# Kernel tuning notes

Hardware: AMD Instinct MI355X
Metric: run time of the kernel (lower is better)

The kernel has to match this reference:

```python
import jax, jax.numpy as jnp
import numpy as np

B, S, DIM, H, DH = 2, 2048, 1024, 16, 64
EPS = 1e-6


def rms_norm(x, w):
    # x: (..., DH); computed in fp32 like the torch module
    norm = jax.lax.rsqrt(jnp.mean(jnp.square(x), axis=-1, keepdims=True) + EPS)
    return (x * norm) * w


def apply_rope(x, freqs):
    # x: (B, H, S, D), freqs: (S, D); torch code slices cos/sin to first half
    d = x.shape[-1] // 2
    cos = jnp.cos(freqs)[None, None, :, :d]
    sin = jnp.sin(freqs)[None, None, :, :d]
    x1, x2 = x[..., :d], x[..., d:]
    return jnp.concatenate([x1 * cos - x2 * sin, x2 * cos + x1 * sin], axis=-1)


def setup_inputs() -> dict:
    key = jax.random.key(0)
    ks = jax.random.split(key, 4)
    x = jax.random.normal(ks[0], (B, S, DIM), dtype=jnp.float32)
    # causal additive mask
    causal = jnp.tril(jnp.ones((S, S), dtype=bool))
    mask = jnp.where(causal, 0.0, -1e9).astype(jnp.float32)[None, None]
    # standard rope frequencies: pos * inv_freq over head_dim
    inv_freq = 1.0 / (10000.0 ** (jnp.arange(0, DH, dtype=jnp.float32) / DH))
    rope_freqs = jnp.arange(S, dtype=jnp.float32)[:, None] * inv_freq[None, :]
    total = H * DH
    w_qkv = jax.random.normal(ks[1], (3 * total, DIM), dtype=jnp.float32) * (DIM ** -0.5)
    w_out = jax.random.normal(ks[2], (DIM, total), dtype=jnp.float32) * (total ** -0.5)
    q_norm_w = jnp.ones((DH,), dtype=jnp.float32)
    k_norm_w = jnp.ones((DH,), dtype=jnp.float32)
    return {"x": x, "mask": mask, "rope_freqs": rope_freqs, "w_qkv": w_qkv,
            "w_out": w_out, "q_norm_w": q_norm_w, "k_norm_w": k_norm_w}


def reference(x, mask, rope_freqs, w_qkv, w_out, q_norm_w, k_norm_w):
    b, s, _ = x.shape
    qkv = (x @ w_qkv.T).reshape(b, s, 3, H, DH)
    q, k, v = qkv[:, :, 0], qkv[:, :, 1], qkv[:, :, 2]
    q = jnp.transpose(rms_norm(q, q_norm_w), (0, 2, 1, 3))  # (B,H,S,DH)
    k = jnp.transpose(rms_norm(k, k_norm_w), (0, 2, 1, 3))
    v = jnp.transpose(v, (0, 2, 1, 3))
    q = apply_rope(q, rope_freqs)
    k = apply_rope(k, rope_freqs)
    scale = DH ** -0.5
    attn = jnp.einsum('bhsd,bhtd->bhst', q, k) * scale + mask
    attn = jax.nn.softmax(attn, axis=-1)
    out = jnp.einsum('bhst,bhtd->bhsd', attn, v)
    out = jnp.transpose(out, (0, 2, 1, 3)).reshape(b, s, H * DH)
    return out @ w_out.T
```

## Files before the change

### kernel.cpp

```cpp
#include <hip/hip_runtime.h>
#include <hip/hip_bf16.h>
#include <stdint.h>

typedef short bf16x8 __attribute__((ext_vector_type(8)));
typedef float f32x4  __attribute__((ext_vector_type(4)));

#define MFMA_BF16(a,b,c) __builtin_amdgcn_mfma_f32_16x16x32_bf16((a),(b),(c),0,0,0)

__device__ __forceinline__ void async_ld16(const void* g, void* l) {
  __builtin_amdgcn_global_load_lds(
      (const __attribute__((address_space(1))) void*)g,
      (__attribute__((address_space(3))) void*)l, 16, 0, 0);
}

__device__ __forceinline__ unsigned short bf16_bits(float x) {
  __hip_bfloat16 h = __float2bfloat16(x);
  return *(unsigned short*)&h;
}

#define NX_C    (2 * 2048 * 1024)
#define NWQKV_C (3072 * 1024)
#define NWOUT_C (1024 * 1024)

__global__ void __launch_bounds__(256)
cvt_all(const float* __restrict__ x, const float* __restrict__ wqkv,
        const float* __restrict__ wout, __hip_bfloat16* __restrict__ dst)
{
  const int i = (blockIdx.x * 256 + threadIdx.x) * 4;
  const float* src;
  int off;
  if (i < NX_C)                { src = x;    off = i; }
  else if (i < NX_C + NWQKV_C) { src = wqkv; off = i - NX_C; }
  else                         { src = wout; off = i - NX_C - NWQKV_C; }
  const float4 v = *(const float4*)(src + off);
  ushort4 u;
  u.x = bf16_bits(v.x); u.y = bf16_bits(v.y);
  u.z = bf16_bits(v.z); u.w = bf16_bits(v.w);
  *(ushort4*)((unsigned short*)dst + i) = u;
}

template<int EPI>
__global__ void __launch_bounds__(256)
gemm_bt(const __hip_bfloat16* __restrict__ A,
        const __hip_bfloat16* __restrict__ B,
        int K,
        __hip_bfloat16* __restrict__ o0,
        __hip_bfloat16* __restrict__ o1,
        __hip_bfloat16* __restrict__ o2,
        float* __restrict__ of)
{
  __shared__ __align__(16) __hip_bfloat16 As[128 * 64];
  __shared__ __align__(16) __hip_bfloat16 Bs[128 * 64];

  const int tid  = threadIdx.x;
  const int w    = tid >> 6;
  const int lane = tid & 63;
  const int quad = lane >> 4;
  const int l15  = lane & 15;

  const int m0 = blockIdx.y * 128;
  const int n0 = blockIdx.x * 128;

  const int sj = lane >> 3;
  const int sg = ((lane & 7) ^ sj) * 8;

  const int pg0 = (((quad ^ (l15 & 3)) | (((l15 >> 2) & 1) << 2))) * 8;
  const int pg1 = pg0 ^ 32;

  const int wm = (w >> 1) * 64;
  const int wn = (w & 1) * 64;

  f32x4 acc[4][4] = {};

  for (int k0 = 0; k0 < K; k0 += 64) {
    __syncthreads();
#pragma unroll
    for (int j = 0; j < 4; ++j) {
      const int c = w * 4 + j;
      async_ld16(A + (size_t)(m0 + c * 8 + sj) * K + k0 + sg, As + c * 512);
      async_ld16(B + (size_t)(n0 + c * 8 + sj) * K + k0 + sg, Bs + c * 512);
    }
    __syncthreads();

    bf16x8 af[4], bfr[4];
#pragma unroll
    for (int t = 0; t < 4; ++t) {
      af[t]  = *(const bf16x8*)(As + (wm + t * 16 + l15) * 64 + pg0);
      bfr[t] = *(const bf16x8*)(Bs + (wn + t * 16 + l15) * 64 + pg0);
    }
#pragma unroll
    for (int mt = 0; mt < 4; ++mt)
#pragma unroll
      for (int nt = 0; nt < 4; ++nt)
        acc[mt][nt] = MFMA_BF16(af[mt], bfr[nt], acc[mt][nt]);
#pragma unroll
    for (int t = 0; t < 4; ++t) {
      af[t]  = *(const bf16x8*)(As + (wm + t * 16 + l15) * 64 + pg1);
      bfr[t] = *(const bf16x8*)(Bs + (wn + t * 16 + l15) * 64 + pg1);
    }
#pragma unroll
    for (int mt = 0; mt < 4; ++mt)
#pragma unroll
      for (int nt = 0; nt < 4; ++nt)
        acc[mt][nt] = MFMA_BF16(af[mt], bfr[nt], acc[mt][nt]);
  }

  const int ldc = (int)gridDim.x * 128;
#pragma unroll
  for (int mt = 0; mt < 4; ++mt) {
#pragma unroll
    for (int nt = 0; nt < 4; ++nt) {
#pragma unroll
      for (int r = 0; r < 4; ++r) {
        const int m = m0 + wm + mt * 16 + quad * 4 + r;
        const int n = n0 + wn + nt * 16 + l15;
        if (EPI == 0) {
          const __hip_bfloat16 hv = __float2bfloat16(acc[mt][nt][r]);
          const int b = m >> 11, s = m & 2047;
          const int which = n >> 10, rem = n & 1023;
          const int h = rem >> 6, d = rem & 63;
          const int bh = b * 16 + h;
          if (which == 0)      o0[((size_t)(bh * 2048 + s) << 6) + d] = hv;
          else if (which == 1) o1[((size_t)(bh * 2048 + s) << 6) + d] = hv;
          else                 o2[((size_t)(bh * 64 + d) << 11) + s] = hv;
        } else {
          of[(size_t)m * ldc + n] = acc[mt][nt][r];
        }
      }
    }
  }
}

__global__ void __launch_bounds__(256)
norm_rope(__hip_bfloat16* __restrict__ qb,
          __hip_bfloat16* __restrict__ kb,
          const float* __restrict__ freqs,
          const float* __restrict__ qw,
          const float* __restrict__ kw)
{
  const int wid  = blockIdx.x * 4 + (threadIdx.x >> 6);
  const int lane = threadIdx.x & 63;
  const int which = wid >> 16;
  const int idx   = wid & 65535;
  const int s     = idx & 2047;

  __hip_bfloat16* buf = which ? kb : qb;
  const float* wgt = which ? kw : qw;

  const size_t base = (size_t)idx * 64;
  float x = __bfloat162float(buf[base + lane]);
  float ss = x * x;
#pragma unroll
  for (int off = 1; off < 64; off <<= 1) ss += __shfl_xor(ss, off);
  const float scale = rsqrtf(ss * (1.0f / 64.0f) + 1e-6f);
  const float y = x * scale * wgt[lane];

  const float f = freqs[s * 64 + (lane & 31)];
  const float c = cosf(f), sn = sinf(f);
  const float part = __shfl_xor(y, 32);
  float o = (lane < 32) ? (y * c - part * sn) : (y * c + part * sn);
  if (which == 0) o *= 0.125f;
  buf[base + lane] = __float2bfloat16(o);
}

__global__ void __launch_bounds__(256, 2)
attn(const __hip_bfloat16* __restrict__ q,
     const __hip_bfloat16* __restrict__ k,
     const __hip_bfloat16* __restrict__ vt,
     __hip_bfloat16* __restrict__ ao)
{
  __shared__ __align__(16) __hip_bfloat16 Ks[2][64 * 64];
  __shared__ __align__(16) __hip_bfloat16 Vs[2][64 * 64];

  const int tid  = threadIdx.x;
  const int w    = tid >> 6;
  const int lane = tid & 63;
  const int quad = lane >> 4;
  const int l15  = lane & 15;

  const int lin  = blockIdx.x;
  const int c8   = lin & 7;
  const int rest = lin >> 3;
  const int pj   = rest & 15;
  const int bh   = ((rest >> 4) << 3) + c8;
  const int b    = bh >> 4, h = bh & 15;

  const __hip_bfloat16* qb = q  + (size_t)bh * 2048 * 64;
  const __hip_bfloat16* kb = k  + (size_t)bh * 2048 * 64;
  const __hip_bfloat16* vb = vt + (size_t)bh * 64 * 2048;

  const int pr = ((l15 >> 2) * 8) + (l15 & 3);

  const int pgk  = (quad ^ (l15 & 3) ^ (((l15 >> 2) & 1) << 2)) * 8;
  const int pgk4 = pgk ^ 32;
  const int pgv  = (quad ^ (l15 & 7)) * 8;
  const int pgv4 = pgv ^ 32;

  const int sj  = lane >> 3;
  const int sp  = lane & 7;
  const int kgA = (sp ^ (sj & 3)) * 8;
  const int kgB = kgA ^ 32;
  const int vgs = (sp ^ sj) * 8;
  const int ck0 = w * 2, ck1 = w * 2 + 1;

#define STAGE(KEY0, BUF) do {                                                     \
    __hip_bfloat16* ks_ = &Ks[BUF][0];                                            \
    __hip_bfloat16* vs_ = &Vs[BUF][0];                                            \
    async_ld16(kb + (size_t)((KEY0) + ck0 * 8 + sj) * 64 + kgA, ks_ + ck0 * 512); \
    async_ld16(kb + (size_t)((KEY0) + ck1 * 8 + sj) * 64 + kgB, ks_ + ck1 * 512); \
    async_ld16(vb + (size_t)(ck0 * 8 + sj) * 2048 + (KEY0) + vgs, vs_ + ck0 * 512); \
    async_ld16(vb + (size_t)(ck1 * 8 + sj) * 2048 + (KEY0) + vgs, vs_ + ck1 * 512); \
  } while (0)

  for (int pass = 0; pass < 2; ++pass) {
    const int J  = pass ? (31 - pj) : pj;
    const int q0 = J * 64 + w * 16;
    const int qi = q0 + l15;

    const bf16x8 bq0 = *(const bf16x8*)(qb + (size_t)qi * 64 + quad * 8);
    const bf16x8 bq1 = *(const bf16x8*)(qb + (size_t)qi * 64 + 32 + quad * 8);

    f32x4 o[4] = {};
    float lsum = 0.f;

    const int ntile = J + 1;

    __syncthreads();
    STAGE(0, 0);

    for (int kt = 0; kt < ntile; ++kt) {
      const int cur = kt & 1;
      const int t0 = kt * 64;

      __syncthreads();
      if (kt + 1 < ntile) STAGE(t0 + 64, cur ^ 1);

      const __hip_bfloat16* Kc = &Ks[cur][0];
      const __hip_bfloat16* Vc = &Vs[cur][0];

      bf16x8 ka00, ka01, ka10, ka11, kb00, kb01, kb10, kb11;
      ka00 = *(const bf16x8*)(Kc + (pr)      * 64 + pgk);
      ka01 = *(const bf16x8*)(Kc + (pr)      * 64 + pgk4);
      ka10 = *(const bf16x8*)(Kc + (pr + 4)  * 64 + pgk);
      ka11 = *(const bf16x8*)(Kc + (pr + 4)  * 64 + pgk4);
      kb00 = *(const bf16x8*)(Kc + (32 + pr)     * 64 + pgk);
      kb01 = *(const bf16x8*)(Kc + (32 + pr)     * 64 + pgk4);
      kb10 = *(const bf16x8*)(Kc + (32 + pr + 4) * 64 + pgk);
      kb11 = *(const bf16x8*)(Kc + (32 + pr + 4) * 64 + pgk4);

      bf16x8 va[2][4];
#pragma unroll
      for (int dt = 0; dt < 4; ++dt) {
        va[0][dt] = *(const bf16x8*)(Vc + (dt * 16 + l15) * 64 + pgv);
        va[1][dt] = *(const bf16x8*)(Vc + (dt * 16 + l15) * 64 + pgv4);
      }

      f32x4 c00 = {}, c01 = {}, c10 = {}, c11 = {};
      c00 = MFMA_BF16(ka00, bq0, c00); c00 = MFMA_BF16(ka01, bq1, c00);
      c01 = MFMA_BF16(ka10, bq0, c01); c01 = MFMA_BF16(ka11, bq1, c01);
      c10 = MFMA_BF16(kb00, bq0, c10); c10 = MFMA_BF16(kb01, bq1, c10);
      c11 = MFMA_BF16(kb10, bq0, c11); c11 = MFMA_BF16(kb11, bq1, c11);

      float e00[4], e01[4], e10[4], e11[4];
#pragma unroll
      for (int r = 0; r < 4; ++r) {
        e00[r] = c00[r]; e01[r] = c01[r]; e10[r] = c10[r]; e11[r] = c11[r];
      }

      if (kt == ntile - 1) {
#pragma unroll
        for (int r = 0; r < 4; ++r) {
          const int k0v = t0 + 8 * quad + r;
          if (k0v      > qi) e00[r] = -1e30f;
          if (k0v + 4  > qi) e01[r] = -1e30f;
          if (k0v + 32 > qi) e10[r] = -1e30f;
          if (k0v + 36 > qi) e11[r] = -1e30f;
        }
      }

      float rs = 0.f;
#pragma unroll
      for (int r = 0; r < 4; ++r) {
        e00[r] = __expf(e00[r] - 8.0f);
        e01[r] = __expf(e01[r] - 8.0f);
        e10[r] = __expf(e10[r] - 8.0f);
        e11[r] = __expf(e11[r] - 8.0f);
        rs += (e00[r] + e01[r]) + (e10[r] + e11[r]);
      }
      lsum += rs;

      bf16x8 pf0, pf1;
#pragma unroll
      for (int r = 0; r < 4; ++r) {
        pf0[r] = (short)bf16_bits(e00[r]);  pf0[r + 4] = (short)bf16_bits(e01[r]);
        pf1[r] = (short)bf16_bits(e10[r]);  pf1[r + 4] = (short)bf16_bits(e11[r]);
      }

#pragma unroll
      for (int dt = 0; dt < 4; ++dt) {
        o[dt] = MFMA_BF16(va[0][dt], pf0, o[dt]);
        o[dt] = MFMA_BF16(va[1][dt], pf1, o[dt]);
      }
    }

    lsum += __shfl_xor(lsum, 16);
    lsum += __shfl_xor(lsum, 32);

    const float inv = 1.0f / lsum;
    const size_t row = ((size_t)(b * 2048 + qi)) * 1024 + h * 64;
#pragma unroll
    for (int dt = 0; dt < 4; ++dt) {
      ushort4 u;
      u.x = bf16_bits(o[dt][0] * inv);
      u.y = bf16_bits(o[dt][1] * inv);
      u.z = bf16_bits(o[dt][2] * inv);
      u.w = bf16_bits(o[dt][3] * inv);
      *(ushort4*)((unsigned short*)ao + row + dt * 16 + quad * 4) = u;
    }
  }
#undef STAGE
}

extern "C" void kernel_launch(void* const* d_in, const int* in_sizes, int n_in,
                              void* d_out, int out_size, void* d_ws, size_t ws_size,
                              hipStream_t stream)
{
  const float* x    = (const float*)d_in[0];
  const float* rf   = (const float*)d_in[2];
  const float* wqkv = (const float*)d_in[3];
  const float* wout = (const float*)d_in[4];
  const float* qw   = (const float*)d_in[5];
  const float* kw   = (const float*)d_in[6];

  const size_t NE = (size_t)2 * 16 * 2048 * 64;

  __hip_bfloat16* qb  = (__hip_bfloat16*)d_ws;
  __hip_bfloat16* kb  = qb  + NE;
  __hip_bfloat16* vt  = kb  + NE;
  __hip_bfloat16* ao  = vt  + NE;
  __hip_bfloat16* xb  = ao  + NE;
  __hip_bfloat16* wqb = xb  + NX_C;
  __hip_bfloat16* wob = wqb + NWQKV_C;

  cvt_all<<<(NX_C + NWQKV_C + NWOUT_C) / 1024, 256, 0, stream>>>(x, wqkv, wout, xb);

  gemm_bt<0><<<dim3(24, 32), 256, 0, stream>>>(xb, wqb, 1024, qb, kb, vt, nullptr);
  norm_rope<<<32768, 256, 0, stream>>>(qb, kb, rf, qw, kw);
  attn<<<512, 256, 0, stream>>>(qb, kb, vt, ao);
  gemm_bt<1><<<dim3(8, 32), 256, 0, stream>>>(ao, wob, 1024,
                                              nullptr, nullptr, nullptr, (float*)d_out);
}
```

Before: 216.4 us.

## Fuse RMSNorm and RoPE into QKV GEMM epilogue and double-buffer K tiles

Removes the separate norm_rope kernel by computing per-head RMS norm, weight scaling, query scaling and rotary embedding directly on the QKV GEMM accumulators before writing bf16 Q/K. This avoids re-reading and re-writing Q/K and one kernel launch. The GEMM main loop also changes from single-buffered 64-wide K steps to double-buffered 32-wide steps, prefetching the next tile asynchronously while computing on the current one. Fast __sincosf replaces cosf/sinf, and the norm is now applied to fp32 accumulators instead of bf16-rounded values, which slightly changes numerics.

```diff
diff --git a/kernel.cpp b/kernel.cpp
--- a/kernel.cpp
+++ b/kernel.cpp
@@ -47,10 +47,13 @@
         __hip_bfloat16* __restrict__ o0,
         __hip_bfloat16* __restrict__ o1,
         __hip_bfloat16* __restrict__ o2,
-        float* __restrict__ of)
+        float* __restrict__ of,
+        const float* __restrict__ freqs,
+        const float* __restrict__ qw,
+        const float* __restrict__ kw)
 {
-  __shared__ __align__(16) __hip_bfloat16 As[128 * 64];
-  __shared__ __align__(16) __hip_bfloat16 Bs[128 * 64];
+  __shared__ __align__(16) __hip_bfloat16 As[2][128 * 32];
+  __shared__ __align__(16) __hip_bfloat16 Bs[2][128 * 32];
 
   const int tid  = threadIdx.x;
   const int w    = tid >> 6;
@@ -61,106 +64,119 @@
   const int m0 = blockIdx.y * 128;
   const int n0 = blockIdx.x * 128;
 
-  const int sj = lane >> 3;
-  const int sg = ((lane & 7) ^ sj) * 8;
-
-  const int pg0 = (((quad ^ (l15 & 3)) | (((l15 >> 2) & 1) << 2))) * 8;
-  const int pg1 = pg0 ^ 32;
+  const int rj = lane >> 2;
+  const int sg = ((lane & 3) ^ (rj & 3)) * 8;
+  const int c0 = w * 2, c1 = w * 2 + 1;
+
+  const int pg = (quad ^ (l15 & 3)) * 8;
 
   const int wm = (w >> 1) * 64;
   const int wn = (w & 1) * 64;
 
   f32x4 acc[4][4] = {};
 
-  for (int k0 = 0; k0 < K; k0 += 64) {
+  async_ld16(A + (size_t)(m0 + c0 * 16 + rj) * K + sg, &As[0][0] + c0 * 512);
+  async_ld16(A + (size_t)(m0 + c1 * 16 + rj) * K + sg, &As[0][0] + c1 * 512);
+  async_ld16(B + (size_t)(n0 + c0 * 16 + rj) * K + sg, &Bs[0][0] + c0 * 512);
+  async_ld16(B + (size_t)(n0 + c1 * 16 + rj) * K + sg, &Bs[0][0] + c1 * 512);
+
+  const int niter = K >> 5;
+  for (int it = 0; it < niter; ++it) {
+    const int cur = it & 1;
     __syncthreads();
-#pragma unroll
-    for (int j = 0; j < 4; ++j) {
-      const int c = w * 4 + j;
-      async_ld16(A + (size_t)(m0 + c * 8 + sj) * K + k0 + sg, As + c * 512);
-      async_ld16(B + (size_t)(n0 + c * 8 + sj) * K + k0 + sg, Bs + c * 512);
-    }
-    __syncthreads();
-
+    if (it + 1 < niter) {
+      const int kn = (it + 1) << 5;
+      async_ld16(A + (size_t)(m0 + c0 * 16 + rj) * K + kn + sg, &As[cur ^ 1][0] + c0 * 512);
+      async_ld16(A + (size_t)(m0 + c1 * 16 + rj) * K + kn + sg, &As[cur ^ 1][0] + c1 * 512);
+      async_ld16(B + (size_t)(n0 + c0 * 16 + rj) * K + kn + sg, &Bs[cur ^ 1][0] + c0 * 512);
+      async_ld16(B + (size_t)(n0 + c1 * 16 + rj) * K + kn + sg, &Bs[cur ^ 1][0] + c1 * 512);
+    }
+
+    const __hip_bfloat16* Ac = &As[cur][0];
+    const __hip_bfloat16* Bc = &Bs[cur][0];
     bf16x8 af[4], bfr[4];
 #pragma unroll
     for (int t = 0; t < 4; ++t) {
-      af[t]  = *(const bf16x8*)(As + (wm + t * 16 + l15) * 64 + pg0);
-      bfr[t] = *(const bf16x8*)(Bs + (wn + t * 16 + l15) * 64 + pg0);
+      af[t]  = *(const bf16x8*)(Ac + (wm + t * 16 + l15) * 32 + pg);
+      bfr[t] = *(const bf16x8*)(Bc + (wn + t * 16 + l15) * 32 + pg);
     }
 #pragma unroll
     for (int mt = 0; mt < 4; ++mt)
 #pragma unroll
       for (int nt = 0; nt < 4; ++nt)
         acc[mt][nt] = MFMA_BF16(af[mt], bfr[nt], acc[mt][nt]);
-#pragma unroll
-    for (int t = 0; t < 4; ++t) {
-      af[t]  = *(const bf16x8*)(As + (wm + t * 16 + l15) * 64 + pg1);
-      bfr[t] = *(const bf16x8*)(Bs + (wn + t * 16 + l15) * 64 + pg1);
-    }
+  }
+
+  if (EPI == 1) {
+    const int ldc = (int)gridDim.x * 128;
 #pragma unroll
     for (int mt = 0; mt < 4; ++mt)
 #pragma unroll
       for (int nt = 0; nt < 4; ++nt)
-        acc[mt][nt] = MFMA_BF16(af[mt], bfr[nt], acc[mt][nt]);
-  }
-
-  const int ldc = (int)gridDim.x * 128;
+#pragma unroll
+        for (int r = 0; r < 4; ++r)
+          of[(size_t)(m0 + wm + mt * 16 + quad * 4 + r) * ldc
+             + n0 + wn + nt * 16 + l15] = acc[mt][nt][r];
+    return;
+  }
+
+  const int which = n0 >> 10;
+  const int hb    = ((n0 & 1023) >> 6) + (wn >> 6);
+
+  if (which == 2) {
+#pragma unroll
+    for (int mt = 0; mt < 4; ++mt)
+#pragma unroll
+      for (int nt = 0; nt < 4; ++nt)
+#pragma unroll
+        for (int r = 0; r < 4; ++r) {
+          const int m = m0 + wm + mt * 16 + quad * 4 + r;
+          const int b = m >> 11, s = m & 2047;
+          const int d = nt * 16 + l15;
+          o2[((size_t)((b * 16 + hb) * 64 + d) << 11) + s] =
+              __float2bfloat16(acc[mt][nt][r]);
+        }
+    return;
+  }
+
+  const float* wgt = which ? kw : qw;
+  __hip_bfloat16* dst = which ? o1 : o0;
+  const float wv0 = wgt[l15], wv1 = wgt[16 + l15];
+  const float wv2 = wgt[32 + l15], wv3 = wgt[48 + l15];
+
 #pragma unroll
   for (int mt = 0; mt < 4; ++mt) {
 #pragma unroll
-    for (int nt = 0; nt < 4; ++nt) {
-#pragma unroll
-      for (int r = 0; r < 4; ++r) {
-        const int m = m0 + wm + mt * 16 + quad * 4 + r;
-        const int n = n0 + wn + nt * 16 + l15;
-        if (EPI == 0) {
-          const __hip_bfloat16 hv = __float2bfloat16(acc[mt][nt][r]);
-          const int b = m >> 11, s = m & 2047;
-          const int which = n >> 10, rem = n & 1023;
-          const int h = rem >> 6, d = rem & 63;
-          const int bh = b * 16 + h;
-          if (which == 0)      o0[((size_t)(bh * 2048 + s) << 6) + d] = hv;
-          else if (which == 1) o1[((size_t)(bh * 2048 + s) << 6) + d] = hv;
-          else                 o2[((size_t)(bh * 64 + d) << 11) + s] = hv;
-        } else {
-          of[(size_t)m * ldc + n] = acc[mt][nt][r];
-        }
-      }
-    }
-  }
-}
-
-__global__ void __launch_bounds__(256)
-norm_rope(__hip_bfloat16* __restrict__ qb,
-          __hip_bfloat16* __restrict__ kb,
-          const float* __restrict__ freqs,
-          const float* __restrict__ qw,
-          const float* __restrict__ kw)
-{
-  const int wid  = blockIdx.x * 4 + (threadIdx.x >> 6);
-  const int lane = threadIdx.x & 63;
-  const int which = wid >> 16;
-  const int idx   = wid & 65535;
-  const int s     = idx & 2047;
-
-  __hip_bfloat16* buf = which ? kb : qb;
-  const float* wgt = which ? kw : qw;
-
-  const size_t base = (size_t)idx * 64;
-  float x = __bfloat162float(buf[base + lane]);
-  float ss = x * x;
-#pragma unroll
-  for (int off = 1; off < 64; off <<= 1) ss += __shfl_xor(ss, off);
-  const float scale = rsqrtf(ss * (1.0f / 64.0f) + 1e-6f);
-  const float y = x * scale * wgt[lane];
-
-  const float f = freqs[s * 64 + (lane & 31)];
-  const float c = cosf(f), sn = sinf(f);
-  const float part = __shfl_xor(y, 32);
-  float o = (lane < 32) ? (y * c - part * sn) : (y * c + part * sn);
-  if (which == 0) o *= 0.125f;
-  buf[base + lane] = __float2bfloat16(o);
+    for (int r = 0; r < 4; ++r) {
+      float ssq = acc[mt][0][r] * acc[mt][0][r] + acc[mt][1][r] * acc[mt][1][r]
+                + acc[mt][2][r] * acc[mt][2][r] + acc[mt][3][r] * acc[mt][3][r];
+      ssq += __shfl_xor(ssq, 1);
+      ssq += __shfl_xor(ssq, 2);
+      ssq += __shfl_xor(ssq, 4);
+      ssq += __shfl_xor(ssq, 8);
+      float sc = rsqrtf(ssq * (1.0f / 64.0f) + 1e-6f);
+      if (which == 0) sc *= 0.125f;
+
+      const float y0 = acc[mt][0][r] * sc * wv0;
+      const float y1 = acc[mt][1][r] * sc * wv1;
+      const float y2 = acc[mt][2][r] * sc * wv2;
+      const float y3 = acc[mt][3][r] * sc * wv3;
+
+      const int m = m0 + wm + mt * 16 + quad * 4 + r;
+      const int b = m >> 11, s = m & 2047;
+      const float f0 = freqs[s * 64 + l15];
+      const float f1 = freqs[s * 64 + 16 + l15];
+      float sn0, cs0, sn1, cs1;
+      __sincosf(f0, &sn0, &cs0);
+      __sincosf(f1, &sn1, &cs1);
+
+      const size_t row = ((size_t)((b * 16 + hb) * 2048 + s)) << 6;
+      dst[row + l15]      = __float2bfloat16(y0 * cs0 - y2 * sn0);
+      dst[row + 16 + l15] = __float2bfloat16(y1 * cs1 - y3 * sn1);
+      dst[row + 32 + l15] = __float2bfloat16(y2 * cs0 + y0 * sn0);
+      dst[row + 48 + l15] = __float2bfloat16(y3 * cs1 + y1 * sn1);
+    }
+  }
 }
 
 __global__ void __launch_bounds__(256, 2)
@@ -344,9 +360,10 @@
 
   cvt_all<<<(NX_C + NWQKV_C + NWOUT_C) / 1024, 256, 0, stream>>>(x, wqkv, wout, xb);
 
-  gemm_bt<0><<<dim3(24, 32), 256, 0, stream>>>(xb, wqb, 1024, qb, kb, vt, nullptr);
-  norm_rope<<<32768, 256, 0, stream>>>(qb, kb, rf, qw, kw);
+  gemm_bt<0><<<dim3(24, 32), 256, 0, stream>>>(xb, wqb, 1024, qb, kb, vt,
+                                               nullptr, rf, qw, kw);
   attn<<<512, 256, 0, stream>>>(qb, kb, vt, ao);
   gemm_bt<1><<<dim3(8, 32), 256, 0, stream>>>(ao, wob, 1024,
-                                              nullptr, nullptr, nullptr, (float*)d_out);
-}
+                                              nullptr, nullptr, nullptr, (float*)d_out,
+                                              nullptr, nullptr, nullptr);
+}
```

New measurement: 191.5 us. 1.13x faster.
